# Optimization experiments

Measured on AMD Instinct MI355X. Metric: run time of the kernel, lower is better.

The kernel has to match this reference:

```python
import jax, jax.numpy as jnp
import numpy as np

N = 50000
E = 800000
D_IN = 1000
D_H2 = 128  # h_dim * multiple
D_H = 16


def gat_conv(x, src, dst, W, attn_l, attn_r, bias, n):
    """DGL-style GATConv (no dropout, no activation). Returns [n, H, F]."""
    H, F = attn_l.shape
    feat = (x @ W).reshape(n, H, F)                      # [N,H,F]
    el = jnp.sum(feat * attn_l[None], axis=-1)           # [N,H]
    er = jnp.sum(feat * attn_r[None], axis=-1)           # [N,H]
    e = jax.nn.leaky_relu(el[src] + er[dst], 0.2)        # [E,H]
    emax = jax.ops.segment_max(e, dst, num_segments=n)   # [N,H] per-dst softmax max
    ee = jnp.exp(e - emax[dst])                          # [E,H]
    denom = jax.ops.segment_sum(ee, dst, num_segments=n) # [N,H]
    alpha = ee / denom[dst]                              # [E,H]
    msg = feat[src] * alpha[..., None]                   # [E,H,F]
    out = jax.ops.segment_sum(msg, dst, num_segments=n)  # [N,H,F]
    return out + bias.reshape(1, H, F)


def setup_inputs() -> dict:
    key = jax.random.key(0)
    ks = jax.random.split(key, 24)
    rn = lambda k, shp, s=0.05: (jax.random.normal(k, shp, dtype=jnp.float32) * s)
    inp = {
        "x": rn(ks[0], (N, D_IN), 1.0),
        "src": jax.random.randint(ks[1], (E,), 0, N, dtype=jnp.int32),
        "dst": jax.random.randint(ks[2], (E,), 0, N, dtype=jnp.int32),
        "W1": rn(ks[3], (D_IN, D_H2)),
        "al1": rn(ks[4], (1, D_H2)),
        "ar1": rn(ks[5], (1, D_H2)),
        "b1": jnp.zeros((D_H2,), jnp.float32),
        "W2": rn(ks[6], (D_H2, 2 * D_H2)),
        "al2": rn(ks[7], (2, D_H2)),
        "ar2": rn(ks[8], (2, D_H2)),
        "b2": jnp.zeros((2 * D_H2,), jnp.float32),
        "Wm": rn(ks[9], (D_H2, 2 * D_H)),
        "alm": rn(ks[10], (2, D_H)),
        "arm": rn(ks[11], (2, D_H)),
        "bm": jnp.zeros((2 * D_H,), jnp.float32),
        "Wv": rn(ks[12], (D_H2, 2 * D_H)),
        "alv": rn(ks[13], (2, D_H)),
        "arv": rn(ks[14], (2, D_H)),
        "bv": jnp.zeros((2 * D_H,), jnp.float32),
        "eps": rn(ks[15], (N, D_H), 1.0),
    }
    return inp


def reference(x, src, dst, W1, al1, ar1, b1, W2, al2, ar2, b2,
              Wm, alm, arm, bm, Wv, alv, arv, bv, eps):
    n = x.shape[0]
    o = gat_conv(x, src, dst, W1, al1, ar1, b1, n).mean(-2)           # [N,128]
    o = gat_conv(o, src, dst, W2, al2, ar2, b2, n).mean(-2) + o       # residual
    mean = gat_conv(o, src, dst, Wm, alm, arm, bm, n).mean(-2)        # [N,16]
    var = jnp.exp(gat_conv(o, src, dst, Wv, alv, arv, bv, n).mean(-2))
    z = mean + jnp.sqrt(var) * eps                                    # reparameterize
    return z, mean, var
```

## Files before the change

### kernel.cpp

```cpp
#include <hip/hip_runtime.h>
#include <hip/hip_bf16.h>
#include <math.h>

typedef unsigned short u16;
typedef unsigned int u32;
typedef __attribute__((ext_vector_type(8))) __bf16 bf16x8;
typedef __attribute__((ext_vector_type(4))) float f32x4;
typedef __attribute__((ext_vector_type(4))) u32 u32x4;
typedef __attribute__((ext_vector_type(2))) u32 u32x2;

#define NNODES 50000
#define NEDGES 800000

__device__ __forceinline__ float bf2f(u16 u) {
    union { u32 i; float f; } v; v.i = ((u32)u) << 16; return v.f;
}
__device__ __forceinline__ u16 f2bf(float x) {
    union { float f; u32 i; } v; v.f = x;
    u32 r = v.i + 0x7fffu + ((v.i >> 16) & 1u);
    return (u16)(r >> 16);
}
__device__ __forceinline__ float lrelu(float x) { return x >= 0.f ? x : 0.2f * x; }

__device__ __forceinline__ void gload_lds16(const u16* g, u16* l) {
    __builtin_amdgcn_global_load_lds((const __attribute__((address_space(1))) u32*)g,
                                     (__attribute__((address_space(3))) u32*)l, 16, 0, 0);
}

__global__ __launch_bounds__(256) void k_zero2(int* a, int* b, int count) {
    int i = blockIdx.x * 256 + threadIdx.x;
    if (i < count) { a[i] = 0; b[i] = 0; }
}

__global__ __launch_bounds__(256) void k_count(const int* __restrict__ dst, int* __restrict__ counts, int e) {
    int i = blockIdx.x * 256 + threadIdx.x;
    if (i < e) atomicAdd(&counts[dst[i]], 1);
}

__global__ __launch_bounds__(256) void k_scan1(const int* __restrict__ counts, int* __restrict__ row_ptr,
                                               int* __restrict__ bsums, int n) {
    __shared__ int tmp[256];
    int t = threadIdx.x, i = blockIdx.x * 256 + t;
    int v = (i < n) ? counts[i] : 0;
    tmp[t] = v; __syncthreads();
    for (int off = 1; off < 256; off <<= 1) {
        int x = 0; if (t >= off) x = tmp[t - off];
        __syncthreads(); tmp[t] += x; __syncthreads();
    }
    if (i < n) row_ptr[i] = tmp[t] - v;
    if (t == 255) bsums[blockIdx.x] = tmp[255];
}

__global__ __launch_bounds__(256) void k_scan2(int* bsums, int nb) {
    __shared__ int tmp[256];
    int t = threadIdx.x;
    int v = (t < nb) ? bsums[t] : 0;
    tmp[t] = v; __syncthreads();
    for (int off = 1; off < 256; off <<= 1) {
        int x = 0; if (t >= off) x = tmp[t - off];
        __syncthreads(); tmp[t] += x; __syncthreads();
    }
    if (t < nb) bsums[t] = tmp[t] - v;
}

__global__ __launch_bounds__(256) void k_scan3(int* __restrict__ row_ptr, const int* __restrict__ bsums,
                                               int n, int total) {
    int i = blockIdx.x * 256 + threadIdx.x;
    if (i < n) row_ptr[i] += bsums[blockIdx.x];
    if (i == 0) row_ptr[n] = total;
}

__global__ __launch_bounds__(256) void k_fill(const int* __restrict__ src, const int* __restrict__ dst,
                                              const int* __restrict__ row_ptr, int* __restrict__ cursor,
                                              int* __restrict__ esrc, int e) {
    int i = blockIdx.x * 256 + threadIdx.x;
    if (i < e) {
        int d = dst[i];
        int p = row_ptr[d] + atomicAdd(&cursor[d], 1);
        esrc[p] = src[i];
    }
}

__global__ __launch_bounds__(256) void k_prep(const float* __restrict__ W1, const float* __restrict__ W2,
                                              const float* __restrict__ Wm, const float* __restrict__ Wv,
                                              const float* __restrict__ al2, const float* __restrict__ ar2,
                                              const float* __restrict__ b2,
                                              u16* __restrict__ W1t, u16* __restrict__ Wct,
                                              u16* __restrict__ Bmvt,
                                              float* __restrict__ ul, float* __restrict__ ur,
                                              float* __restrict__ bmean) {
    int b = blockIdx.x, t = threadIdx.x;
    if (b < 500) {
        int i = b * 256 + t;
        int k = i >> 7, n = i & 127;
        W1t[(size_t)n * 1000 + k] = f2bf(W1[i]);
    } else if (b < 628) {
        int i = (b - 500) * 256 + t;
        int f = i >> 8, c = i & 255, h = c >> 7, k = c & 127;
        Wct[i] = f2bf(0.5f * W2[(size_t)k * 256 + h * 128 + f]);
    } else if (b == 628) {
        int h = t >> 7, k = t & 127;
        const float* wrow = W2 + (size_t)k * 256 + h * 128;
        const float* alh = al2 + h * 128;
        const float* arh = ar2 + h * 128;
        float sl = 0.f, sr = 0.f;
        for (int f = 0; f < 128; f += 4) {
            f32x4 w = *(const f32x4*)(wrow + f);
            f32x4 a = *(const f32x4*)(alh + f);
            f32x4 r = *(const f32x4*)(arh + f);
#pragma unroll
            for (int q = 0; q < 4; q++) { sl += w[q] * a[q]; sr += w[q] * r[q]; }
        }
        ul[t] = sl; ur[t] = sr;
        if (t < 128) bmean[t] = 0.5f * (b2[t] + b2[128 + t]);
    } else {
        for (int i = t; i < 64 * 128; i += 256) {
            int c = i >> 7, k = i & 127;
            Bmvt[i] = f2bf(c < 32 ? Wm[(size_t)k * 32 + c] : Wv[(size_t)k * 32 + (c - 32)]);
        }
    }
}

__device__ __forceinline__ void load_af(const float* __restrict__ arow, int k0, int K, bf16x8& a) {
    if (k0 + 8 <= K) {
        f32x4 a0 = *(const f32x4*)(arow + k0);
        f32x4 a1 = *(const f32x4*)(arow + k0 + 4);
#pragma unroll
        for (int j = 0; j < 4; j++) { a[j] = (__bf16)a0[j]; a[4 + j] = (__bf16)a1[j]; }
    } else {
#pragma unroll
        for (int j = 0; j < 8; j++) a[j] = (__bf16)0.f;
    }
}
__device__ __forceinline__ void load_af(const u16* __restrict__ arow, int k0, int K, bf16x8& a) {
    if (k0 + 8 <= K) a = *(const bf16x8*)(arow + k0);
    else {
#pragma unroll
        for (int j = 0; j < 8; j++) a[j] = (__bf16)0.f;
    }
}

template <typename AT, int MODE>
__global__ __launch_bounds__(256) void k_gemm_tiled(const AT* __restrict__ A, const u16* __restrict__ Bt,
                                                    u16* __restrict__ C, int M, int Nn, int K,
                                                    const float* __restrict__ bias,
                                                    const u16* __restrict__ resid,
                                                    const float* __restrict__ al,
                                                    const float* __restrict__ ar,
                                                    float* __restrict__ el, float* __restrict__ er) {
    __shared__ __align__(16) u16 lb[2][4096];
    const int tid = threadIdx.x;
    const int wave = tid >> 6, lane = tid & 63;
    const int m = lane & 15, quad = lane >> 4;
    const int row0 = blockIdx.x * 64 + wave * 16;
    const int col0 = blockIdx.y * 128;

    f32x4 acc[8];
#pragma unroll
    for (int t = 0; t < 8; t++)
#pragma unroll
        for (int r = 0; r < 4; r++) acc[t][r] = 0.f;

    int arr = row0 + m; if (arr > M - 1) arr = M - 1;
    const AT* arow = A + (size_t)arr * K;
    const int colA = (wave & 1) * 64 + lane;
    const int qb = (wave >> 1) * 2;
    const u16* bcol = Bt + (size_t)(col0 + colA) * K;
    u16* lds0 = &lb[0][(qb * 128 + colA) * 8];
    u16* lds1 = &lb[1][(qb * 128 + colA) * 8];

    const int nsteps = (K + 31) >> 5;

#pragma unroll
    for (int p = 0; p < 2; ++p)
        gload_lds16(bcol + (qb + p) * 8, lds0 + p * 1024);
    bf16x8 acur, anext;
    load_af(arow, quad * 8, K, acur);
    __syncthreads();

    for (int s = 0; s < nsteps; ++s) {
        const int buf = s & 1;
        if (s + 1 < nsteps) {
            const int k0n = (s + 1) * 32;
            load_af(arow, k0n + quad * 8, K, anext);
            u16* ldsn = buf ? lds0 : lds1;
#pragma unroll
            for (int p = 0; p < 2; ++p) {
                int kq = k0n + (qb + p) * 8;
                if (kq < K) gload_lds16(bcol + kq, ldsn + p * 1024);
            }
        }
#pragma unroll
        for (int t = 0; t < 8; ++t) {
            bf16x8 b = *(const bf16x8*)&lb[buf][(quad * 128 + t * 16 + m) * 8];
            acc[t] = __builtin_amdgcn_mfma_f32_16x16x32_bf16(acur, b, acc[t], 0, 0, 0);
        }
        acur = anext;
        __syncthreads();
    }

#pragma unroll
    for (int r = 0; r < 4; r++) {
        int row = row0 + quad * 4 + r;
        if (MODE == 0) {
            float pe = 0.f, pr = 0.f;
#pragma unroll
            for (int t = 0; t < 8; t++) {
                float a = acc[t][r];
                int c = col0 + t * 16 + m;
                pe += a * al[c]; pr += a * ar[c];
            }
#pragma unroll
            for (int off = 8; off; off >>= 1) { pe += __shfl_xor(pe, off); pr += __shfl_xor(pr, off); }
            if (m == 0 && row < M) { el[row] = pe; er[row] = pr; }
        }
#pragma unroll
        for (int t = 0; t < 8; t++) {
            int col = col0 + t * 16 + m;
            if (row < M) {
                float v = acc[t][r];
                if (MODE == 1) v += bias[col] + bf2f(resid[(size_t)row * Nn + col]);
                C[(size_t)row * Nn + col] = f2bf(v);
            }
        }
    }
}

__global__ __launch_bounds__(64) void k_gemmmv(const u16* __restrict__ A, const u16* __restrict__ Bt,
                                               u16* __restrict__ featmv,
                                               const float* __restrict__ alm, const float* __restrict__ arm,
                                               const float* __restrict__ alv, const float* __restrict__ arv,
                                               float* __restrict__ elm, float* __restrict__ erm,
                                               float* __restrict__ elv, float* __restrict__ erv, int M) {
    int row0 = blockIdx.x * 16;
    int lane = threadIdx.x;
    int m = lane & 15, quad = lane >> 4;
    f32x4 acc[4];
#pragma unroll
    for (int t = 0; t < 4; t++)
#pragma unroll
        for (int r = 0; r < 4; r++) acc[t][r] = 0.f;

    const u16* arow = A + (size_t)(row0 + m) * 128 + quad * 8;
#pragma unroll
    for (int s = 0; s < 4; ++s) {
        bf16x8 a = *(const bf16x8*)(arow + s * 32);
#pragma unroll
        for (int t = 0; t < 4; t++) {
            bf16x8 b = *(const bf16x8*)(Bt + (size_t)(t * 16 + m) * 128 + s * 32 + quad * 8);
            acc[t] = __builtin_amdgcn_mfma_f32_16x16x32_bf16(a, b, acc[t], 0, 0, 0);
        }
    }
#pragma unroll
    for (int r = 0; r < 4; r++) {
        int row = row0 + quad * 4 + r;
#pragma unroll
        for (int t = 0; t < 4; t++) {
            float a = acc[t][r];
            const float* alp = (t < 2) ? alm : alv;
            const float* arp = (t < 2) ? arm : arv;
            float pe = a * alp[(t & 1) * 16 + m];
            float pr = a * arp[(t & 1) * 16 + m];
#pragma unroll
            for (int off = 8; off; off >>= 1) { pe += __shfl_xor(pe, off); pr += __shfl_xor(pr, off); }
            if (m == 0 && row < M) {
                float* elp = (t < 2) ? elm : elv;
                float* erp = (t < 2) ? erm : erv;
                elp[row * 2 + (t & 1)] = pe; erp[row * 2 + (t & 1)] = pr;
            }
            if (row < M) featmv[(size_t)row * 64 + t * 16 + m] = f2bf(a);
        }
    }
}

__global__ __launch_bounds__(256) void k_agg1(const int* __restrict__ row_ptr, const int* __restrict__ esrc,
                                              const u16* __restrict__ feat, const float* __restrict__ el,
                                              const float* __restrict__ er, const float* __restrict__ bias,
                                              const float* __restrict__ ul, const float* __restrict__ ur,
                                              u16* __restrict__ o_bf, float* __restrict__ el2,
                                              float* __restrict__ er2, int n) {
    int wave = threadIdx.x >> 6, lane = threadIdx.x & 63;
    int l = lane & 31;
    int node = blockIdx.x * 8 + wave * 2 + (lane >> 5);
    if (node >= n) node = n - 1;
    int beg = row_ptr[node], deg = row_ptr[node + 1] - beg;
    float erd = er[node];
    int degmax = max(deg, __shfl_xor(deg, 32));
    const int srcb = lane & 32;
    float acc0 = 0.f, acc1 = 0.f, acc2 = 0.f, acc3 = 0.f, den = 0.f;
    for (int off0 = 0; off0 < degmax; off0 += 32) {
        float w = 0.f; int s = 0;
        if (off0 + l < deg) { s = esrc[beg + off0 + l]; w = expf(lrelu(el[s] + erd)); }
        den += w;
        int cnt = min(32, degmax - off0);
        int j = 0;
        for (; j + 4 <= cnt; j += 4) {
            int s0 = __shfl(s, srcb + j),     s1 = __shfl(s, srcb + j + 1);
            int s2 = __shfl(s, srcb + j + 2), s3 = __shfl(s, srcb + j + 3);
            float w0 = __shfl(w, srcb + j),     w1 = __shfl(w, srcb + j + 1);
            float w2 = __shfl(w, srcb + j + 2), w3 = __shfl(w, srcb + j + 3);
            u32x2 p0 = ((const u32x2*)(feat + (size_t)s0 * 128))[l];
            u32x2 p1 = ((const u32x2*)(feat + (size_t)s1 * 128))[l];
            u32x2 p2 = ((const u32x2*)(feat + (size_t)s2 * 128))[l];
            u32x2 p3 = ((const u32x2*)(feat + (size_t)s3 * 128))[l];
            acc0 += w0 * bf2f((u16)(p0.x & 0xffff)) + w1 * bf2f((u16)(p1.x & 0xffff))
                  + w2 * bf2f((u16)(p2.x & 0xffff)) + w3 * bf2f((u16)(p3.x & 0xffff));
            acc1 += w0 * bf2f((u16)(p0.x >> 16)) + w1 * bf2f((u16)(p1.x >> 16))
                  + w2 * bf2f((u16)(p2.x >> 16)) + w3 * bf2f((u16)(p3.x >> 16));
            acc2 += w0 * bf2f((u16)(p0.y & 0xffff)) + w1 * bf2f((u16)(p1.y & 0xffff))
                  + w2 * bf2f((u16)(p2.y & 0xffff)) + w3 * bf2f((u16)(p3.y & 0xffff));
            acc3 += w0 * bf2f((u16)(p0.y >> 16)) + w1 * bf2f((u16)(p1.y >> 16))
                  + w2 * bf2f((u16)(p2.y >> 16)) + w3 * bf2f((u16)(p3.y >> 16));
        }
        for (; j < cnt; ++j) {
            int sj = __shfl(s, srcb + j);
            float wj = __shfl(w, srcb + j);
            u32x2 pv = ((const u32x2*)(feat + (size_t)sj * 128))[l];
            acc0 += wj * bf2f((u16)(pv.x & 0xffff));
            acc1 += wj * bf2f((u16)(pv.x >> 16));
            acc2 += wj * bf2f((u16)(pv.y & 0xffff));
            acc3 += wj * bf2f((u16)(pv.y >> 16));
        }
    }
#pragma unroll
    for (int off = 16; off; off >>= 1) den += __shfl_xor(den, off);
    float inv = (den > 0.f) ? 1.f / den : 0.f;
    const int c0 = 4 * l;
    float o0 = acc0 * inv + bias[c0];
    float o1 = acc1 * inv + bias[c0 + 1];
    float o2 = acc2 * inv + bias[c0 + 2];
    float o3 = acc3 * inv + bias[c0 + 3];
#pragma unroll
    for (int h = 0; h < 2; ++h) {
        const float* ulh = ul + h * 128 + c0;
        const float* urh = ur + h * 128 + c0;
        float pe = o0 * ulh[0] + o1 * ulh[1] + o2 * ulh[2] + o3 * ulh[3];
        float pr = o0 * urh[0] + o1 * urh[1] + o2 * urh[2] + o3 * urh[3];
#pragma unroll
        for (int off = 16; off; off >>= 1) { pe += __shfl_xor(pe, off); pr += __shfl_xor(pr, off); }
        if (l == 0) { el2[node * 2 + h] = pe; er2[node * 2 + h] = pr; }
    }
    u32x2 pv;
    pv.x = (u32)f2bf(o0) | ((u32)f2bf(o1) << 16);
    pv.y = (u32)f2bf(o2) | ((u32)f2bf(o3) << 16);
    ((u32x2*)(o_bf + (size_t)node * 128))[l] = pv;
}

__global__ __launch_bounds__(256) void k_agg2o(const int* __restrict__ row_ptr, const int* __restrict__ esrc,
                                               const u16* __restrict__ o_in, const float* __restrict__ el,
                                               const float* __restrict__ er, u16* __restrict__ agg, int n) {
    int wave = threadIdx.x >> 6, lane = threadIdx.x & 63;
    int l = lane & 31;
    int node = blockIdx.x * 8 + wave * 2 + (lane >> 5);
    if (node >= n) node = n - 1;
    int beg = row_ptr[node], deg = row_ptr[node + 1] - beg;
    float er0 = er[node * 2], er1 = er[node * 2 + 1];
    int degmax = max(deg, __shfl_xor(deg, 32));
    const int srcb = lane & 32;
    float a00 = 0.f, a01 = 0.f, a02 = 0.f, a03 = 0.f;
    float a10 = 0.f, a11 = 0.f, a12 = 0.f, a13 = 0.f;
    float d0 = 0.f, d1 = 0.f;
    for (int off0 = 0; off0 < degmax; off0 += 32) {
        float w0 = 0.f, w1 = 0.f; int s = 0;
        if (off0 + l < deg) {
            s = esrc[beg + off0 + l];
            float2 e2 = *(const float2*)(el + 2 * s);
            w0 = expf(lrelu(e2.x + er0));
            w1 = expf(lrelu(e2.y + er1));
        }
        d0 += w0; d1 += w1;
        int cnt = min(32, degmax - off0);
        int j = 0;
        for (; j + 4 <= cnt; j += 4) {
            int sa = __shfl(s, srcb + j),     sb = __shfl(s, srcb + j + 1);
            int sc = __shfl(s, srcb + j + 2), sd = __shfl(s, srcb + j + 3);
            float w0a = __shfl(w0, srcb + j),     w0b = __shfl(w0, srcb + j + 1);
            float w0c = __shfl(w0, srcb + j + 2), w0d = __shfl(w0, srcb + j + 3);
            float w1a = __shfl(w1, srcb + j),     w1b = __shfl(w1, srcb + j + 1);
            float w1c = __shfl(w1, srcb + j + 2), w1d = __shfl(w1, srcb + j + 3);
            u32x2 pa = ((const u32x2*)(o_in + (size_t)sa * 128))[l];
            u32x2 pb = ((const u32x2*)(o_in + (size_t)sb * 128))[l];
            u32x2 pc = ((const u32x2*)(o_in + (size_t)sc * 128))[l];
            u32x2 pd = ((const u32x2*)(o_in + (size_t)sd * 128))[l];
            float fa0 = bf2f((u16)(pa.x & 0xffff)), fa1 = bf2f((u16)(pa.x >> 16));
            float fa2 = bf2f((u16)(pa.y & 0xffff)), fa3 = bf2f((u16)(pa.y >> 16));
            float fb0 = bf2f((u16)(pb.x & 0xffff)), fb1 = bf2f((u16)(pb.x >> 16));
            float fb2 = bf2f((u16)(pb.y & 0xffff)), fb3 = bf2f((u16)(pb.y >> 16));
            float fc0 = bf2f((u16)(pc.x & 0xffff)), fc1 = bf2f((u16)(pc.x >> 16));
            float fc2 = bf2f((u16)(pc.y & 0xffff)), fc3 = bf2f((u16)(pc.y >> 16));
            float fd0 = bf2f((u16)(pd.x & 0xffff)), fd1 = bf2f((u16)(pd.x >> 16));
            float fd2 = bf2f((u16)(pd.y & 0xffff)), fd3 = bf2f((u16)(pd.y >> 16));
            a00 += w0a * fa0 + w0b * fb0 + w0c * fc0 + w0d * fd0;
            a01 += w0a * fa1 + w0b * fb1 + w0c * fc1 + w0d * fd1;
            a02 += w0a * fa2 + w0b * fb2 + w0c * fc2 + w0d * fd2;
            a03 += w0a * fa3 + w0b * fb3 + w0c * fc3 + w0d * fd3;
            a10 += w1a * fa0 + w1b * fb0 + w1c * fc0 + w1d * fd0;
            a11 += w1a * fa1 + w1b * fb1 + w1c * fc1 + w1d * fd1;
            a12 += w1a * fa2 + w1b * fb2 + w1c * fc2 + w1d * fd2;
            a13 += w1a * fa3 + w1b * fb3 + w1c * fc3 + w1d * fd3;
        }
        for (; j < cnt; ++j) {
            int sj = __shfl(s, srcb + j);
            float w0j = __shfl(w0, srcb + j), w1j = __shfl(w1, srcb + j);
            u32x2 pv = ((const u32x2*)(o_in + (size_t)sj * 128))[l];
            float f0 = bf2f((u16)(pv.x & 0xffff)), f1 = bf2f((u16)(pv.x >> 16));
            float f2 = bf2f((u16)(pv.y & 0xffff)), f3 = bf2f((u16)(pv.y >> 16));
            a00 += w0j * f0; a01 += w0j * f1; a02 += w0j * f2; a03 += w0j * f3;
            a10 += w1j * f0; a11 += w1j * f1; a12 += w1j * f2; a13 += w1j * f3;
        }
    }
#pragma unroll
    for (int off = 16; off; off >>= 1) { d0 += __shfl_xor(d0, off); d1 += __shfl_xor(d1, off); }
    float i0 = (d0 > 0.f) ? 1.f / d0 : 0.f, i1 = (d1 > 0.f) ? 1.f / d1 : 0.f;
    u32x2 p0, p1;
    p0.x = (u32)f2bf(a00 * i0) | ((u32)f2bf(a01 * i0) << 16);
    p0.y = (u32)f2bf(a02 * i0) | ((u32)f2bf(a03 * i0) << 16);
    p1.x = (u32)f2bf(a10 * i1) | ((u32)f2bf(a11 * i1) << 16);
    p1.y = (u32)f2bf(a12 * i1) | ((u32)f2bf(a13 * i1) << 16);
    u32x2* aw = (u32x2*)(agg + (size_t)node * 256);
    aw[l] = p0;
    aw[32 + l] = p1;
}

__global__ __launch_bounds__(256) void k_aggmv(const int* __restrict__ row_ptr, const int* __restrict__ esrc,
                                               const u16* __restrict__ featmv,
                                               const float* __restrict__ elm, const float* __restrict__ erm,
                                               const float* __restrict__ elv, const float* __restrict__ erv,
                                               const float* __restrict__ bm, const float* __restrict__ bv,
                                               const float* __restrict__ eps, float* __restrict__ out, int n) {
    __shared__ float wsm[256 * 4];
    __shared__ int ssm[256];
    int tid = threadIdx.x;
    int wave = tid >> 6, lane = tid & 63;
    int l = lane & 31;
    int node = blockIdx.x * 8 + wave * 2 + (lane >> 5);
    if (node >= n) node = n - 1;
    int tbl = l >> 4, h = (l >> 3) & 1;
    const int wtype = l >> 3;
    int beg = row_ptr[node], deg = row_ptr[node + 1] - beg;
    float erm0 = erm[2 * node], erm1 = erm[2 * node + 1];
    float erv0 = erv[2 * node], erv1 = erv[2 * node + 1];
    int degmax = max(deg, __shfl_xor(deg, 32));
    const int bidx = wave * 64 + (lane & 32);
    float acc0 = 0.f, acc1 = 0.f;
    float dm0 = 0.f, dm1 = 0.f, dv0 = 0.f, dv1 = 0.f;
    for (int off0 = 0; off0 < degmax; off0 += 32) {
        float wm0 = 0.f, wm1 = 0.f, wv0 = 0.f, wv1 = 0.f; int s = 0;
        if (off0 + l < deg) {
            s = esrc[beg + off0 + l];
            float2 em = *(const float2*)(elm + 2 * s);
            float2 ev = *(const float2*)(elv + 2 * s);
            wm0 = expf(lrelu(em.x + erm0));
            wm1 = expf(lrelu(em.y + erm1));
            wv0 = expf(lrelu(ev.x + erv0));
            wv1 = expf(lrelu(ev.y + erv1));
        }
        dm0 += wm0; dm1 += wm1; dv0 += wv0; dv1 += wv1;
        f32x4 wq; wq[0] = wm0; wq[1] = wm1; wq[2] = wv0; wq[3] = wv1;
        *(f32x4*)&wsm[tid * 4] = wq;
        ssm[tid] = s;
        int cnt = min(32, degmax - off0);
        int j = 0;
        for (; j + 2 <= cnt; j += 2) {
            int sa = ssm[bidx + j], sb = ssm[bidx + j + 1];
            float wa = wsm[(bidx + j) * 4 + wtype];
            float wb = wsm[(bidx + j + 1) * 4 + wtype];
            u32 pa = ((const u32*)(featmv + (size_t)sa * 64))[l];
            u32 pb = ((const u32*)(featmv + (size_t)sb * 64))[l];
            acc0 += wa * bf2f((u16)(pa & 0xffff)) + wb * bf2f((u16)(pb & 0xffff));
            acc1 += wa * bf2f((u16)(pa >> 16)) + wb * bf2f((u16)(pb >> 16));
        }
        for (; j < cnt; ++j) {
            int sj = ssm[bidx + j];
            float wj = wsm[(bidx + j) * 4 + wtype];
            u32 pv = ((const u32*)(featmv + (size_t)sj * 64))[l];
            acc0 += wj * bf2f((u16)(pv & 0xffff));
            acc1 += wj * bf2f((u16)(pv >> 16));
        }
    }
#pragma unroll
    for (int off = 16; off; off >>= 1) {
        dm0 += __shfl_xor(dm0, off); dm1 += __shfl_xor(dm1, off);
        dv0 += __shfl_xor(dv0, off); dv1 += __shfl_xor(dv1, off);
    }
    float den = tbl ? (h ? dv1 : dv0) : (h ? dm1 : dm0);
    float inv = (den > 0.f) ? 1.f / den : 0.f;
    const int fidx0 = (2 * l) & 31;
    float bias0 = tbl ? bv[fidx0] : bm[fidx0];
    float bias1 = tbl ? bv[fidx0 + 1] : bm[fidx0 + 1];
    float outc0 = acc0 * inv + bias0;
    float outc1 = acc1 * inv + bias1;
    float hm0 = 0.5f * (outc0 + __shfl_xor(outc0, 8));
    float hm1 = 0.5f * (outc1 + __shfl_xor(outc1, 8));
    int srcv = (lane & 32) + 16 + (l & 7);
    float vp0 = __shfl(hm0, srcv);
    float vp1 = __shfl(hm1, srcv);
    if (l < 8) {
        int f0 = 2 * l;
        float var0 = expf(vp0), var1 = expf(vp1);
        float2 e2 = *(const float2*)(eps + (size_t)node * 16 + f0);
        float z0 = hm0 + sqrtf(var0) * e2.x;
        float z1 = hm1 + sqrtf(var1) * e2.y;
        size_t base = (size_t)node * 16 + f0;
        *(float2*)(out + base) = make_float2(z0, z1);
        *(float2*)(out + (size_t)NNODES * 16 + base) = make_float2(hm0, hm1);
        *(float2*)(out + (size_t)2 * NNODES * 16 + base) = make_float2(var0, var1);
    }
}

extern "C" void kernel_launch(void* const* d_in, const int* in_sizes, int n_in,
                              void* d_out, int out_size, void* d_ws, size_t ws_size,
                              hipStream_t stream) {
    const int N = NNODES, E = NEDGES;
    const float* x   = (const float*)d_in[0];
    const int* src   = (const int*)d_in[1];
    const int* dst   = (const int*)d_in[2];
    const float* W1  = (const float*)d_in[3];
    const float* al1 = (const float*)d_in[4];
    const float* ar1 = (const float*)d_in[5];
    const float* b1  = (const float*)d_in[6];
    const float* W2  = (const float*)d_in[7];
    const float* al2 = (const float*)d_in[8];
    const float* ar2 = (const float*)d_in[9];
    const float* b2  = (const float*)d_in[10];
    const float* Wm  = (const float*)d_in[11];
    const float* alm = (const float*)d_in[12];
    const float* arm = (const float*)d_in[13];
    const float* bm  = (const float*)d_in[14];
    const float* Wv  = (const float*)d_in[15];
    const float* alv = (const float*)d_in[16];
    const float* arv = (const float*)d_in[17];
    const float* bv  = (const float*)d_in[18];
    const float* eps = (const float*)d_in[19];
    float* out = (float*)d_out;

    char* ws = (char*)d_ws;
    size_t off = 0;
    auto take = [&](size_t bytes) { size_t r = off; off += (bytes + 255) & ~(size_t)255; return r; };
    int* counts   = (int*)(ws + take((size_t)N * 4));
    int* cursor   = (int*)(ws + take((size_t)N * 4));
    int* row_ptr  = (int*)(ws + take((size_t)(N + 1) * 4));
    int* bsums    = (int*)(ws + take(256 * 4));
    int* esrc     = (int*)(ws + take((size_t)E * 4));
    u16* W1t      = (u16*)(ws + take((size_t)128 * 1000 * 2));
    u16* Wct      = (u16*)(ws + take((size_t)128 * 256 * 2));
    u16* Bmvt     = (u16*)(ws + take((size_t)64 * 128 * 2));
    float* ul2    = (float*)(ws + take(256 * 4));
    float* ur2    = (float*)(ws + take(256 * 4));
    float* bmean  = (float*)(ws + take(128 * 4));
    float* el1    = (float*)(ws + take((size_t)N * 4));
    float* er1    = (float*)(ws + take((size_t)N * 4));
    float* el2    = (float*)(ws + take((size_t)N * 2 * 4));
    float* er2    = (float*)(ws + take((size_t)N * 2 * 4));
    float* elm    = (float*)(ws + take((size_t)N * 2 * 4));
    float* erm    = (float*)(ws + take((size_t)N * 2 * 4));
    float* elv    = (float*)(ws + take((size_t)N * 2 * 4));
    float* erv    = (float*)(ws + take((size_t)N * 2 * 4));
    u16* o_bf     = (u16*)(ws + take((size_t)N * 128 * 2));
    u16* o2_bf    = (u16*)(ws + take((size_t)N * 128 * 2));
    u16* R        = (u16*)(ws + take((size_t)N * 256 * 2));
    u16* feat1    = R;
    u16* agg      = R;
    u16* featmv   = R;
    (void)ws_size; (void)n_in; (void)in_sizes; (void)out_size;

    const int nb = (N + 255) / 256;
    const int eb = (E + 255) / 256;
    const int wb8 = (N + 7) / 8;
    const int gb = (N + 63) / 64;

    k_prep<<<dim3(630), 256, 0, stream>>>(W1, W2, Wm, Wv, al2, ar2, b2, W1t, Wct, Bmvt, ul2, ur2, bmean);

    k_zero2<<<dim3(nb), 256, 0, stream>>>(counts, cursor, N);
    k_count<<<dim3(eb), 256, 0, stream>>>(dst, counts, E);
    k_scan1<<<dim3(nb), 256, 0, stream>>>(counts, row_ptr, bsums, N);
    k_scan2<<<dim3(1), 256, 0, stream>>>(bsums, nb);
    k_scan3<<<dim3(nb), 256, 0, stream>>>(row_ptr, bsums, N, E);
    k_fill<<<dim3(eb), 256, 0, stream>>>(src, dst, row_ptr, cursor, esrc, E);

    k_gemm_tiled<float, 0><<<dim3(gb, 1), 256, 0, stream>>>(x, W1t, feat1, N, 128, 1000,
                                                            nullptr, nullptr, al1, ar1, el1, er1);
    k_agg1<<<dim3(wb8), 256, 0, stream>>>(row_ptr, esrc, feat1, el1, er1, b1, ul2, ur2,
                                          o_bf, el2, er2, N);

    k_agg2o<<<dim3(wb8), 256, 0, stream>>>(row_ptr, esrc, o_bf, el2, er2, agg, N);
    k_gemm_tiled<u16, 1><<<dim3(gb, 1), 256, 0, stream>>>(agg, Wct, o2_bf, N, 128, 256,
                                                          bmean, o_bf, nullptr, nullptr, nullptr, nullptr);

    k_gemmmv<<<dim3(N / 16), 64, 0, stream>>>(o2_bf, Bmvt, featmv, alm, arm, alv, arv,
                                              elm, erm, elv, erv, N);
    k_aggmv<<<dim3(wb8), 256, 0, stream>>>(row_ptr, esrc, featmv, elm, erm, elv, erv,
                                           bm, bv, eps, out, N);
}
```

Measured before the change: 577.5 us.

## Stage B in 256-wide K chunks per barrier instead of 32-wide double buffer

```diff
diff --git a/kernel.cpp b/kernel.cpp
--- a/kernel.cpp
+++ b/kernel.cpp
@@ -148,12 +148,11 @@
                                                     const float* __restrict__ al,
                                                     const float* __restrict__ ar,
                                                     float* __restrict__ el, float* __restrict__ er) {
-    __shared__ __align__(16) u16 lb[2][4096];
+    __shared__ __align__(16) u16 lb[32 * 128 * 8];
     const int tid = threadIdx.x;
     const int wave = tid >> 6, lane = tid & 63;
     const int m = lane & 15, quad = lane >> 4;
     const int row0 = blockIdx.x * 64 + wave * 16;
-    const int col0 = blockIdx.y * 128;
 
     f32x4 acc[8];
 #pragma unroll
@@ -163,39 +162,33 @@
 
     int arr = row0 + m; if (arr > M - 1) arr = M - 1;
     const AT* arow = A + (size_t)arr * K;
-    const int colA = (wave & 1) * 64 + lane;
-    const int qb = (wave >> 1) * 2;
-    const u16* bcol = Bt + (size_t)(col0 + colA) * K;
-    u16* lds0 = &lb[0][(qb * 128 + colA) * 8];
-    u16* lds1 = &lb[1][(qb * 128 + colA) * 8];
-
-    const int nsteps = (K + 31) >> 5;
-
-#pragma unroll
-    for (int p = 0; p < 2; ++p)
-        gload_lds16(bcol + (qb + p) * 8, lds0 + p * 1024);
-    bf16x8 acur, anext;
-    load_af(arow, quad * 8, K, acur);
-    __syncthreads();
-
-    for (int s = 0; s < nsteps; ++s) {
-        const int buf = s & 1;
-        if (s + 1 < nsteps) {
-            const int k0n = (s + 1) * 32;
-            load_af(arow, k0n + quad * 8, K, anext);
-            u16* ldsn = buf ? lds0 : lds1;
-#pragma unroll
-            for (int p = 0; p < 2; ++p) {
-                int kq = k0n + (qb + p) * 8;
-                if (kq < K) gload_lds16(bcol + kq, ldsn + p * 1024);
+    const int scol = tid & 127, shi = tid >> 7;
+    const u16* bcol = Bt + (size_t)scol * K;
+    u16* sdst = &lb[((size_t)shi * 128 + scol) * 8];
+
+    const int KC = 256;
+    const int nchunks = (K + KC - 1) / KC;
+    bf16x8 afr[8];
+
+    for (int c = 0; c < nchunks; ++c) {
+        const int kb = c * KC;
+#pragma unroll
+        for (int ks = 0; ks < 8; ++ks)
+            load_af(arow, kb + ks * 32 + quad * 8, K, afr[ks]);
+#pragma unroll
+        for (int it = 0; it < 16; ++it) {
+            int kq = kb + (it * 2 + shi) * 8;
+            if (kq < K) gload_lds16(bcol + kq, sdst + it * 2048);
+        }
+        __syncthreads();
+#pragma unroll
+        for (int ks = 0; ks < 8; ++ks) {
+#pragma unroll
+            for (int t = 0; t < 8; ++t) {
+                bf16x8 b = *(const bf16x8*)&lb[((ks * 4 + quad) * 128 + t * 16 + m) * 8];
+                acc[t] = __builtin_amdgcn_mfma_f32_16x16x32_bf16(afr[ks], b, acc[t], 0, 0, 0);
             }
         }
-#pragma unroll
-        for (int t = 0; t < 8; ++t) {
-            bf16x8 b = *(const bf16x8*)&lb[buf][(quad * 128 + t * 16 + m) * 8];
-            acc[t] = __builtin_amdgcn_mfma_f32_16x16x32_bf16(acur, b, acc[t], 0, 0, 0);
-        }
-        acur = anext;
         __syncthreads();
     }
 
@@ -207,7 +200,7 @@
 #pragma unroll
             for (int t = 0; t < 8; t++) {
                 float a = acc[t][r];
-                int c = col0 + t * 16 + m;
+                int c = t * 16 + m;
                 pe += a * al[c]; pr += a * ar[c];
             }
 #pragma unroll
@@ -216,7 +209,7 @@
         }
 #pragma unroll
         for (int t = 0; t < 8; t++) {
-            int col = col0 + t * 16 + m;
+            int col = t * 16 + m;
             if (row < M) {
                 float v = acc[t][r];
                 if (MODE == 1) v += bias[col] + bf2f(resid[(size_t)row * Nn + col]);
@@ -578,14 +571,14 @@
     k_scan3<<<dim3(nb), 256, 0, stream>>>(row_ptr, bsums, N, E);
     k_fill<<<dim3(eb), 256, 0, stream>>>(src, dst, row_ptr, cursor, esrc, E);
 
-    k_gemm_tiled<float, 0><<<dim3(gb, 1), 256, 0, stream>>>(x, W1t, feat1, N, 128, 1000,
-                                                            nullptr, nullptr, al1, ar1, el1, er1);
+    k_gemm_tiled<float, 0><<<dim3(gb), 256, 0, stream>>>(x, W1t, feat1, N, 128, 1000,
+                                                         nullptr, nullptr, al1, ar1, el1, er1);
     k_agg1<<<dim3(wb8), 256, 0, stream>>>(row_ptr, esrc, feat1, el1, er1, b1, ul2, ur2,
                                           o_bf, el2, er2, N);
 
     k_agg2o<<<dim3(wb8), 256, 0, stream>>>(row_ptr, esrc, o_bf, el2, er2, agg, N);
-    k_gemm_tiled<u16, 1><<<dim3(gb, 1), 256, 0, stream>>>(agg, Wct, o2_bf, N, 128, 256,
-                                                          bmean, o_bf, nullptr, nullptr, nullptr, nullptr);
+    k_gemm_tiled<u16, 1><<<dim3(gb), 256, 0, stream>>>(agg, Wct, o2_bf, N, 128, 256,
+                                                       bmean, o_bf, nullptr, nullptr, nullptr, nullptr);
 
     k_gemmmv<<<dim3(N / 16), 64, 0, stream>>>(o2_bf, Bmvt, featmv, alm, arm, alv, arv,
                                               elm, erm, elv, erv, N);
```

Result: no change. 579.2 us (+0.3%).
